# Kernel tuning notes

Hardware: AMD Instinct MI355X
Metric: run time of the kernel (lower is better)

Reference implementation:

```python
import jax, jax.numpy as jnp
import numpy as np

SL, BS, E, H, PF, STRIDE, SHIFT = 2048, 2, 1024, 16, 16, 1, 0
DH = E // H  # 64


def setup_inputs() -> dict:
    key = jax.random.key(0)
    ks = jax.random.split(key, 6)
    s = 0.02
    return {
        'x': jax.random.normal(ks[0], (SL, BS, E), jnp.float32),
        'ln_g': jnp.ones((E,), jnp.float32),
        'ln_b': jnp.zeros((E,), jnp.float32),
        'Wq': jax.random.normal(ks[1], (E, E), jnp.float32) * s,
        'bq': jnp.zeros((E,), jnp.float32),
        'Wk': jax.random.normal(ks[2], (E, E), jnp.float32) * s,
        'bk': jnp.zeros((E,), jnp.float32),
        'Wv': jax.random.normal(ks[3], (E, E), jnp.float32) * s,
        'bv': jnp.zeros((E,), jnp.float32),
        'Wo': jax.random.normal(ks[4], (E, E), jnp.float32) * s,
        'bo': jnp.zeros((E,), jnp.float32),
    }


def _layernorm(x, g, b, eps=1e-5):
    m = x.mean(-1, keepdims=True)
    v = jnp.var(x, axis=-1, keepdims=True)
    return (x - m) * jax.lax.rsqrt(v + eps) * g + b


def _sparsify(context, h):
    # faithful to sparsify(): r = (arange(h)+1)*stride - pf + shift (+ arange(pf)), mod c
    c = context.shape[0]
    base = (jnp.arange(h) + 1) * STRIDE - PF + SHIFT          # [h]
    idx = (base[None, :] + jnp.arange(PF)[:, None]) % c       # [pf, h]
    return context[idx.reshape(-1)].reshape(PF, h, context.shape[1], context.shape[2])


def reference(x, ln_g, ln_b, Wq, bq, Wk, bk, Wv, bv, Wo, bo):
    sl, bs, e = x.shape
    residual = x
    xn = _layernorm(x, ln_g, ln_b)
    # gather pf-sized local context window per query position (modular wrap)
    fetch = _sparsify(xn, sl)                                  # [pf, sl, bs, E]
    # per-token query (length-1) attending to its pf gathered keys
    q = (xn @ Wq + bq).reshape(sl, bs, H, DH)                  # [sl,bs,H,dh]
    k = (fetch @ Wk + bk).reshape(PF, sl, bs, H, DH)           # [pf,sl,bs,H,dh]
    v = (fetch @ Wv + bv).reshape(PF, sl, bs, H, DH)
    scale = 1.0 / jnp.sqrt(jnp.float32(DH))
    scores = jnp.einsum('sbhd,psbhd->sbhp', q, k) * scale      # [sl,bs,H,pf]
    attn = jax.nn.softmax(scores, axis=-1)
    out = jnp.einsum('sbhp,psbhd->sbhd', attn, v).reshape(sl, bs, e)
    out = out @ Wo + bo                                        # output projection
    # dropout is a no-op in eval
    return residual + out
```

## Files before the change

### kernel.cpp

```cpp
#include <hip/hip_runtime.h>
#include <cstdint>
#include <cstddef>

#define SLEN 2048
#define BSZ  2
#define EDIM 1024
#define NHEAD 16
#define DHEAD 64
#define PFW  16
#define NTOK (SLEN*BSZ)

#define BK 32

typedef __attribute__((ext_vector_type(8))) short short8;
typedef __attribute__((ext_vector_type(4))) float floatx4;
typedef __attribute__((ext_vector_type(4))) int   int4v;

__device__ __forceinline__ short f2bf(float f) {
  union { float f; uint32_t u; } v; v.f = f;
  uint32_t r = v.u + 0x7fffu + ((v.u >> 16) & 1u);
  return (short)(r >> 16);
}
__device__ __forceinline__ float bf2f(short s) {
  union { uint32_t u; float f; } v; v.u = ((uint32_t)(uint16_t)s) << 16;
  return v.f;
}
__device__ __forceinline__ int q8(float f, float inv) {
  int q = __float2int_rn(f * inv);
  return min(127, max(-127, q));
}

__device__ __forceinline__ void async16(const void* g, void* l) {
  __builtin_amdgcn_global_load_lds((const __attribute__((address_space(1))) void*)g,
                                   (__attribute__((address_space(3))) void*)l,
                                   16, 0, 0);
}

__global__ __launch_bounds__(256) void prep_kernel(
    const float* __restrict__ x, const float* __restrict__ g,
    const float* __restrict__ b, char* __restrict__ xn_i8,
    float* __restrict__ xn_scl,
    const float* __restrict__ W0, const float* __restrict__ W1,
    const float* __restrict__ W2, const float* __restrict__ W3,
    short* __restrict__ Wt_base)
{
  const int bid = blockIdx.x;
  const int tid = threadIdx.x;

  if (bid < NTOK) {
    const int row = bid;
    const float4 v = ((const float4*)(x + (size_t)row * EDIM))[tid];
    float s  = v.x + v.y + v.z + v.w;
    float ss = v.x * v.x + v.y * v.y + v.z * v.z + v.w * v.w;
#pragma unroll
    for (int off = 32; off; off >>= 1) {
      s  += __shfl_xor(s, off);
      ss += __shfl_xor(ss, off);
    }
    __shared__ float ws_s[4], ws_ss[4], ws_m[4];
    const int lane = tid & 63, wave = tid >> 6;
    if (lane == 0) { ws_s[wave] = s; ws_ss[wave] = ss; }
    __syncthreads();
    s  = ws_s[0] + ws_s[1] + ws_s[2] + ws_s[3];
    ss = ws_ss[0] + ws_ss[1] + ws_ss[2] + ws_ss[3];

    const float mean = s * (1.0f / EDIM);
    const float var  = ss * (1.0f / EDIM) - mean * mean;
    const float rs   = rsqrtf(var + 1e-5f);

    const float4 gv = ((const float4*)g)[tid];
    const float4 bv = ((const float4*)b)[tid];
    const float n0 = (v.x - mean) * rs * gv.x + bv.x;
    const float n1 = (v.y - mean) * rs * gv.y + bv.y;
    const float n2 = (v.z - mean) * rs * gv.z + bv.z;
    const float n3 = (v.w - mean) * rs * gv.w + bv.w;

    float am = fmaxf(fmaxf(fabsf(n0), fabsf(n1)), fmaxf(fabsf(n2), fabsf(n3)));
#pragma unroll
    for (int off = 32; off; off >>= 1) am = fmaxf(am, __shfl_xor(am, off));
    if (lane == 0) ws_m[wave] = am;
    __syncthreads();
    am = fmaxf(fmaxf(ws_m[0], ws_m[1]), fmaxf(ws_m[2], ws_m[3]));

    const float inv = (am > 1e-30f) ? 127.0f / am : 0.0f;
    const int q0 = q8(n0, inv), q1 = q8(n1, inv), q2 = q8(n2, inv), q3 = q8(n3, inv);
    const uint32_t pack = (uint32_t)(q0 & 0xff) | ((uint32_t)(q1 & 0xff) << 8) |
                          ((uint32_t)(q2 & 0xff) << 16) | ((uint32_t)(q3 & 0xff) << 24);
    ((uint32_t*)(xn_i8 + (size_t)row * EDIM))[tid] = pack;
    if (tid == 0) xn_scl[row] = am * (1.0f / 127.0f);
  } else {
    const int t = bid - NTOK;
    const int z = t >> 10;
    const int rem = t & 1023;
    const int n0 = (rem & 31) * 32;
    const int k0 = (rem >> 5) * 32;
    const float* W = (z == 0) ? W0 : (z == 1) ? W1 : (z == 2) ? W2 : W3;
    short* Wt = Wt_base + (size_t)z * EDIM * EDIM;

    __shared__ float tile[32][33];
    const int tx = tid & 31;
    const int ty = tid >> 5;
#pragma unroll
    for (int i = 0; i < 4; ++i)
      tile[ty + i * 8][tx] = W[(size_t)(k0 + ty + i * 8) * EDIM + n0 + tx];
    __syncthreads();
#pragma unroll
    for (int i = 0; i < 4; ++i)
      Wt[(size_t)(n0 + ty + i * 8) * EDIM + k0 + tx] = f2bf(tile[tx][ty + i * 8]);
  }
}

__global__ __launch_bounds__(256) void quant_w(
    const short* __restrict__ Wt, char* __restrict__ w_i8,
    float* __restrict__ w_scl)
{
  const int R = blockIdx.x;
  const int tid = threadIdx.x;
  const short4 s4 = ((const short4*)(Wt + (size_t)R * EDIM))[tid];
  const float w0 = bf2f(s4.x), w1 = bf2f(s4.y), w2 = bf2f(s4.z), w3 = bf2f(s4.w);

  float am = fmaxf(fmaxf(fabsf(w0), fabsf(w1)), fmaxf(fabsf(w2), fabsf(w3)));
#pragma unroll
  for (int off = 32; off; off >>= 1) am = fmaxf(am, __shfl_xor(am, off));
  __shared__ float wm[4];
  const int lane = tid & 63, wave = tid >> 6;
  if (lane == 0) wm[wave] = am;
  __syncthreads();
  am = fmaxf(fmaxf(wm[0], wm[1]), fmaxf(wm[2], wm[3]));

  const float inv = (am > 1e-30f) ? 127.0f / am : 0.0f;
  const int q0 = q8(w0, inv), q1 = q8(w1, inv), q2 = q8(w2, inv), q3 = q8(w3, inv);
  const uint32_t pack = (uint32_t)(q0 & 0xff) | ((uint32_t)(q1 & 0xff) << 8) |
                        ((uint32_t)(q2 & 0xff) << 16) | ((uint32_t)(q3 & 0xff) << 24);
  ((uint32_t*)(w_i8 + (size_t)R * EDIM))[tid] = pack;
  if (tid == 0) w_scl[R] = am * (1.0f / 127.0f);
}

__global__ __launch_bounds__(256) void gemm_qkv_i8(
    const char* __restrict__ xn_i8, const float* __restrict__ xn_scl,
    const char* __restrict__ w_i8, const float* __restrict__ w_scl,
    const float* __restrict__ bq, const float* __restrict__ bk,
    const float* __restrict__ bv, short* __restrict__ qkv_base)
{
  __shared__ __align__(16) char As[128 * 64];
  __shared__ __align__(16) char Bs[128 * 64];

  const int bid  = blockIdx.x;
  const int xcd  = bid & 7;
  const int slot = bid >> 3;
  const int nz   = xcd * 3 + slot / 32;
  const int mt   = slot & 31;
  const int z    = nz >> 3;
  const int nt   = nz & 7;

  const char*  Bt   = w_i8 + (size_t)z * EDIM * EDIM;
  const float* bscl = w_scl + z * EDIM;
  const float* bias = (z == 0) ? bq : (z == 1) ? bk : bv;
  short* out        = qkv_base + (size_t)z * NTOK * EDIM;

  const int bm = mt * 128;
  const int bn = nt * 128;
  const int tid  = threadIdx.x;
  const int lane = tid & 63;
  const int wave = tid >> 6;

  int4v acc[4][4];
#pragma unroll
  for (int i = 0; i < 4; ++i)
#pragma unroll
    for (int j = 0; j < 4; ++j) { int4v zz = {0, 0, 0, 0}; acc[i][j] = zz; }

  const int lrow  = lane >> 2;
  const int lcolB = (lane & 3) * 16;
  const char* gA0 = xn_i8 + (size_t)(bm + wave * 32 + lrow) * EDIM + lcolB;
  const char* gA1 = gA0 + (size_t)16 * EDIM;
  const char* gB0 = Bt + (size_t)(bn + wave * 32 + lrow) * EDIM + lcolB;
  const char* gB1 = gB0 + (size_t)16 * EDIM;
  char* lA0 = As + wave * 2048;
  char* lA1 = lA0 + 1024;
  char* lB0 = Bs + wave * 2048;
  char* lB1 = lB0 + 1024;

  const int wm  = (wave >> 1) * 64;
  const int wn  = (wave & 1) * 64;
  const int fr  = lane & 15;
  const int fqB = (lane >> 4) * 16;

  for (int k0 = 0; k0 < EDIM; k0 += 64) {
    async16(gA0, lA0); async16(gA1, lA1);
    async16(gB0, lB0); async16(gB1, lB1);
    gA0 += 64; gA1 += 64; gB0 += 64; gB1 += 64;
    __syncthreads();

    int4v af[4], bf[4];
#pragma unroll
    for (int mi = 0; mi < 4; ++mi)
      af[mi] = *(const int4v*)(As + (size_t)(wm + mi * 16 + fr) * 64 + fqB);
#pragma unroll
    for (int ni = 0; ni < 4; ++ni)
      bf[ni] = *(const int4v*)(Bs + (size_t)(wn + ni * 16 + fr) * 64 + fqB);
#pragma unroll
    for (int mi = 0; mi < 4; ++mi)
#pragma unroll
      for (int ni = 0; ni < 4; ++ni)
        acc[mi][ni] = __builtin_amdgcn_mfma_i32_16x16x64_i8(
            af[mi], bf[ni], acc[mi][ni], 0, 0, 0);
    __syncthreads();
  }

  const int r0 = bm + wm + ((lane >> 4) * 4);
  const int c0 = bn + wn + (lane & 15);
#pragma unroll
  for (int mi = 0; mi < 4; ++mi) {
    float sa[4];
#pragma unroll
    for (int r = 0; r < 4; ++r) sa[r] = xn_scl[r0 + mi * 16 + r];
#pragma unroll
    for (int ni = 0; ni < 4; ++ni) {
      const int4v v = acc[mi][ni];
      const int col = c0 + ni * 16;
      const float sb = bscl[col];
      const float bb = bias[col];
#pragma unroll
      for (int r = 0; r < 4; ++r) {
        const int row = r0 + mi * 16 + r;
        out[(size_t)row * EDIM + col] = f2bf((float)v[r] * (sa[r] * sb) + bb);
      }
    }
  }
}

__global__ __launch_bounds__(256) void gemm_o(
    const short* __restrict__ Aattn, const short* __restrict__ Wot,
    const float* __restrict__ bo, const float* __restrict__ residual,
    float* __restrict__ out)
{
  __shared__ short As[64 * BK];
  __shared__ short Bs[128 * BK];
  const int bm = blockIdx.x * 64;
  const int bn = blockIdx.y * 128;
  const int tid  = threadIdx.x;
  const int lane = tid & 63;
  const int wave = tid >> 6;

  floatx4 acc[2][4];
#pragma unroll
  for (int i = 0; i < 2; ++i)
#pragma unroll
    for (int j = 0; j < 4; ++j) { floatx4 zz = {0.f, 0.f, 0.f, 0.f}; acc[i][j] = zz; }

  const int lrow = lane >> 2;
  const int lcol = (lane & 3) * 8;
  const short* gA0 = Aattn + (size_t)(bm + wave * 16 + lrow) * EDIM + lcol;
  const short* gB0 = Wot + (size_t)(bn + wave * 32 + lrow) * EDIM + lcol;
  const short* gB1 = gB0 + (size_t)16 * EDIM;
  short* lA0 = As + wave * 512;
  short* lB0 = Bs + wave * 1024;
  short* lB1 = lB0 + 512;

  const int wm = (wave >> 1) * 32;
  const int wn = (wave & 1) * 64;
  const int fr = lane & 15;
  const int fq = (lane >> 4) * 8;

  for (int k0 = 0; k0 < EDIM; k0 += BK) {
    async16(gA0, lA0);
    async16(gB0, lB0); async16(gB1, lB1);
    gA0 += BK; gB0 += BK; gB1 += BK;
    __syncthreads();

    short8 af[2], bf[4];
#pragma unroll
    for (int mi = 0; mi < 2; ++mi)
      af[mi] = *(const short8*)(As + (size_t)(wm + mi * 16 + fr) * BK + fq);
#pragma unroll
    for (int ni = 0; ni < 4; ++ni)
      bf[ni] = *(const short8*)(Bs + (size_t)(wn + ni * 16 + fr) * BK + fq);
#pragma unroll
    for (int mi = 0; mi < 2; ++mi)
#pragma unroll
      for (int ni = 0; ni < 4; ++ni)
        acc[mi][ni] = __builtin_amdgcn_mfma_f32_16x16x32_bf16(
            af[mi], bf[ni], acc[mi][ni], 0, 0, 0);
    __syncthreads();
  }

  const int r0 = bm + wm + ((lane >> 4) * 4);
  const int c0 = bn + wn + (lane & 15);
#pragma unroll
  for (int mi = 0; mi < 2; ++mi)
#pragma unroll
    for (int ni = 0; ni < 4; ++ni) {
      const floatx4 v = acc[mi][ni];
      const int col = c0 + ni * 16;
      const float bb = bo[col];
#pragma unroll
      for (int r = 0; r < 4; ++r) {
        const int row = r0 + mi * 16 + r;
        const size_t idx = (size_t)row * EDIM + col;
        out[idx] = residual[idx] + v[r] + bb;
      }
    }
}

#define VT_LD 80
#define PB_LD 40

__global__ __launch_bounds__(256) void attn_mfma(
    const short* __restrict__ Q, const short* __restrict__ K,
    const short* __restrict__ V, short* __restrict__ O)
{
  const int tid  = threadIdx.x;
  const int lane = tid & 63;
  const int wave = tid >> 6;
  const int quad = lane >> 4;
  const int l16  = lane & 15;

  const int bh = blockIdx.y;
  const int h  = bh & (NHEAD - 1);
  const int b  = bh >> 4;
  const int s_blk = blockIdx.x * 64;
  const int col0  = h * DHEAD;

  __shared__ __align__(16) short VT[64 * VT_LD];
  __shared__ __align__(16) short Pb[4][16 * PB_LD];

  for (int task = tid; task < 320; task += 256) {
    const int kp  = task >> 3;
    const int dg  = task & 7;
    const int kk0 = kp * 2;
    int sA = s_blk - 15 + kk0;
    int sB = sA + 1;
    if (sA < 0) sA += SLEN;  if (sA >= SLEN) sA -= SLEN;
    if (sB < 0) sB += SLEN;  if (sB >= SLEN) sB -= SLEN;
    const short8 vA = *(const short8*)(V + (size_t)(sA * BSZ + b) * EDIM + col0 + dg * 8);
    const short8 vB = *(const short8*)(V + (size_t)(sB * BSZ + b) * EDIM + col0 + dg * 8);
#pragma unroll
    for (int j = 0; j < 8; ++j) {
      const int d = dg * 8 + j;
      const uint32_t pack = (uint32_t)(uint16_t)vA[j] | ((uint32_t)(uint16_t)vB[j] << 16);
      *(uint32_t*)&VT[d * VT_LD + kk0] = pack;
    }
  }

  const int sw = s_blk + wave * 16;
  short8 aq[2];
  {
    const size_t base = (size_t)((sw + l16) * BSZ + b) * EDIM + col0 + quad * 8;
    aq[0] = *(const short8*)(Q + base);
    aq[1] = *(const short8*)(Q + base + 32);
  }
  short8 bkf[2][2];
#pragma unroll
  for (int T = 0; T < 2; ++T) {
    int ks = sw - 15 + T * 16 + l16;
    if (ks < 0) ks += SLEN;
    if (ks >= SLEN) ks -= SLEN;
    const size_t base = (size_t)(ks * BSZ + b) * EDIM + col0 + quad * 8;
    bkf[T][0] = *(const short8*)(K + base);
    bkf[T][1] = *(const short8*)(K + base + 32);
  }

  floatx4 S[2];
  { floatx4 zz = {0.f, 0.f, 0.f, 0.f}; S[0] = zz; S[1] = zz; }
#pragma unroll
  for (int T = 0; T < 2; ++T) {
    S[T] = __builtin_amdgcn_mfma_f32_16x16x32_bf16(aq[0], bkf[T][0], S[T], 0, 0, 0);
    S[T] = __builtin_amdgcn_mfma_f32_16x16x32_bf16(aq[1], bkf[T][1], S[T], 0, 0, 0);
  }

  float sc[2][4];
#pragma unroll
  for (int T = 0; T < 2; ++T)
#pragma unroll
    for (int r = 0; r < 4; ++r) {
      const int m = quad * 4 + r;
      const int c = T * 16 + l16;
      const int d = c - m;
      sc[T][r] = (d >= 0 && d <= 15) ? S[T][r] * 0.125f : -1e30f;
    }
  float mx[4], sm[4];
#pragma unroll
  for (int r = 0; r < 4; ++r) mx[r] = fmaxf(sc[0][r], sc[1][r]);
#pragma unroll
  for (int off = 1; off <= 8; off <<= 1)
#pragma unroll
    for (int r = 0; r < 4; ++r) mx[r] = fmaxf(mx[r], __shfl_xor(mx[r], off));
  float p[2][4];
#pragma unroll
  for (int r = 0; r < 4; ++r) {
    p[0][r] = __expf(sc[0][r] - mx[r]);
    p[1][r] = __expf(sc[1][r] - mx[r]);
    sm[r] = p[0][r] + p[1][r];
  }
#pragma unroll
  for (int off = 1; off <= 8; off <<= 1)
#pragma unroll
    for (int r = 0; r < 4; ++r) sm[r] += __shfl_xor(sm[r], off);

  __syncthreads();

  short* Pw = Pb[wave];
#pragma unroll
  for (int T = 0; T < 2; ++T)
#pragma unroll
    for (int r = 0; r < 4; ++r) {
      const int m = quad * 4 + r;
      const int c = T * 16 + l16;
      Pw[m * PB_LD + c] = f2bf(p[T][r]);
    }
  __syncthreads();
  const short8 ap = *(const short8*)(Pw + l16 * PB_LD + quad * 8);

  floatx4 Oacc[4];
  { floatx4 zz = {0.f, 0.f, 0.f, 0.f}; Oacc[0] = zz; Oacc[1] = zz; Oacc[2] = zz; Oacc[3] = zz; }
#pragma unroll
  for (int nt = 0; nt < 4; ++nt) {
    const short8 bv = *(const short8*)(VT + (nt * 16 + l16) * VT_LD + wave * 16 + quad * 8);
    Oacc[nt] = __builtin_amdgcn_mfma_f32_16x16x32_bf16(ap, bv, Oacc[nt], 0, 0, 0);
  }

#pragma unroll
  for (int nt = 0; nt < 4; ++nt)
#pragma unroll
    for (int r = 0; r < 4; ++r) {
      const int m = quad * 4 + r;
      const size_t idx = (size_t)((sw + m) * BSZ + b) * EDIM + col0 + nt * 16 + l16;
      O[idx] = f2bf(Oacc[nt][r] / sm[r]);
    }
}

extern "C" void kernel_launch(void* const* d_in, const int* in_sizes, int n_in,
                              void* d_out, int out_size, void* d_ws, size_t ws_size,
                              hipStream_t stream) {
  const float* x    = (const float*)d_in[0];
  const float* ln_g = (const float*)d_in[1];
  const float* ln_b = (const float*)d_in[2];
  const float* Wq   = (const float*)d_in[3];
  const float* bq   = (const float*)d_in[4];
  const float* Wk   = (const float*)d_in[5];
  const float* bk   = (const float*)d_in[6];
  const float* Wv   = (const float*)d_in[7];
  const float* bv   = (const float*)d_in[8];
  const float* Wo   = (const float*)d_in[9];
  const float* bo   = (const float*)d_in[10];
  float* out = (float*)d_out;

  char* ws = (char*)d_ws;
  char*  xn_i8  = ws;
  short* Wt     = (short*)(ws + ((size_t)4  << 20));
  char*  w_i8   = ws + ((size_t)12 << 20);
  short* QKV    = (short*)(ws + ((size_t)15 << 20));
  short* attn   = (short*)(ws + ((size_t)39 << 20));
  float* xn_scl = (float*)(ws + ((size_t)47 << 20));
  float* w_scl  = (float*)(ws + ((size_t)47 << 20) + (1 << 16));

  prep_kernel<<<NTOK + 4096, 256, 0, stream>>>(x, ln_g, ln_b, xn_i8, xn_scl,
                                               Wq, Wk, Wv, Wo, Wt);
  quant_w<<<3 * EDIM, 256, 0, stream>>>(Wt, w_i8, w_scl);
  gemm_qkv_i8<<<768, 256, 0, stream>>>(xn_i8, xn_scl, w_i8, w_scl,
                                       bq, bk, bv, QKV);
  attn_mfma<<<dim3(SLEN / 64, BSZ * NHEAD), 256, 0, stream>>>(
      QKV, QKV + (size_t)NTOK * EDIM, QKV + (size_t)2 * NTOK * EDIM, attn);
  gemm_o<<<dim3(NTOK / 64, EDIM / 128), 256, 0, stream>>>(
      attn, Wt + (size_t)3 * EDIM * EDIM, bo, x, out);
}
```

Before: 153.3 us.

## Quantize attention output to int8 and run output projection with int8 MFMA

The attention kernel now emits per-row, per-head int8 values plus a scale, instead of bf16. The output projection becomes an int8 GEMM using i32 MFMA with a K-tile of 64, which matches one head. Each tile's integer partial is rescaled into a float accumulator, and the quantization of Wo is folded into the existing weight quantizer by extending its grid. The aim is to halve operand bytes and use the faster int8 matrix path, at the cost of extra per-tile dequantization work and lower accuracy.

```diff
diff --git a/kernel.cpp b/kernel.cpp
--- a/kernel.cpp
+++ b/kernel.cpp
@@ -230,75 +230,100 @@
   }
 }
 
-__global__ __launch_bounds__(256) void gemm_o(
-    const short* __restrict__ Aattn, const short* __restrict__ Wot,
+__global__ __launch_bounds__(256) void gemm_o_i8(
+    const char* __restrict__ A8, const float* __restrict__ a_scl,
+    const char* __restrict__ w_i8, const float* __restrict__ w_scl,
     const float* __restrict__ bo, const float* __restrict__ residual,
     float* __restrict__ out)
 {
-  __shared__ short As[64 * BK];
-  __shared__ short Bs[128 * BK];
+  __shared__ __align__(16) char As[64 * 64];
+  __shared__ __align__(16) char Bs[128 * 64];
+  __shared__ float sa_lds[64 * 17];
+
   const int bm = blockIdx.x * 64;
   const int bn = blockIdx.y * 128;
   const int tid  = threadIdx.x;
   const int lane = tid & 63;
   const int wave = tid >> 6;
 
-  floatx4 acc[2][4];
+#pragma unroll
+  for (int i = 0; i < 4; ++i) {
+    const int e = tid + i * 256;
+    const int row = e >> 4, h = e & 15;
+    sa_lds[row * 17 + h] = a_scl[(size_t)(bm + row) * NHEAD + h];
+  }
+
+  floatx4 facc[2][4];
 #pragma unroll
   for (int i = 0; i < 2; ++i)
 #pragma unroll
-    for (int j = 0; j < 4; ++j) { floatx4 zz = {0.f, 0.f, 0.f, 0.f}; acc[i][j] = zz; }
-
-  const int lrow = lane >> 2;
-  const int lcol = (lane & 3) * 8;
-  const short* gA0 = Aattn + (size_t)(bm + wave * 16 + lrow) * EDIM + lcol;
-  const short* gB0 = Wot + (size_t)(bn + wave * 32 + lrow) * EDIM + lcol;
-  const short* gB1 = gB0 + (size_t)16 * EDIM;
-  short* lA0 = As + wave * 512;
-  short* lB0 = Bs + wave * 1024;
-  short* lB1 = lB0 + 512;
-
-  const int wm = (wave >> 1) * 32;
-  const int wn = (wave & 1) * 64;
-  const int fr = lane & 15;
-  const int fq = (lane >> 4) * 8;
-
-  for (int k0 = 0; k0 < EDIM; k0 += BK) {
+    for (int j = 0; j < 4; ++j) { floatx4 zz = {0.f, 0.f, 0.f, 0.f}; facc[i][j] = zz; }
+
+  const int lrow  = lane >> 2;
+  const int lcolB = (lane & 3) * 16;
+  const char* gA0 = A8 + (size_t)(bm + wave * 16 + lrow) * EDIM + lcolB;
+  const char* gB0 = w_i8 + (size_t)3 * EDIM * EDIM +
+                    (size_t)(bn + wave * 32 + lrow) * EDIM + lcolB;
+  const char* gB1 = gB0 + (size_t)16 * EDIM;
+  char* lA0 = As + wave * 1024;
+  char* lB0 = Bs + wave * 2048;
+  char* lB1 = lB0 + 1024;
+
+  const int wm  = (wave >> 1) * 32;
+  const int wn  = (wave & 1) * 64;
+  const int fr  = lane & 15;
+  const int fqB = (lane >> 4) * 16;
+  const int q4  = lane >> 4;
+
+  for (int ki = 0; ki < 16; ++ki) {
     async16(gA0, lA0);
     async16(gB0, lB0); async16(gB1, lB1);
-    gA0 += BK; gB0 += BK; gB1 += BK;
-    __syncthreads();
-
-    short8 af[2], bf[4];
+    gA0 += 64; gB0 += 64; gB1 += 64;
+    __syncthreads();
+
+    int4v af[2], bf[4];
 #pragma unroll
     for (int mi = 0; mi < 2; ++mi)
-      af[mi] = *(const short8*)(As + (size_t)(wm + mi * 16 + fr) * BK + fq);
+      af[mi] = *(const int4v*)(As + (size_t)(wm + mi * 16 + fr) * 64 + fqB);
 #pragma unroll
     for (int ni = 0; ni < 4; ++ni)
-      bf[ni] = *(const short8*)(Bs + (size_t)(wn + ni * 16 + fr) * BK + fq);
+      bf[ni] = *(const int4v*)(Bs + (size_t)(wn + ni * 16 + fr) * 64 + fqB);
+
+    float sa_v[2][4];
 #pragma unroll
     for (int mi = 0; mi < 2; ++mi)
 #pragma unroll
-      for (int ni = 0; ni < 4; ++ni)
-        acc[mi][ni] = __builtin_amdgcn_mfma_f32_16x16x32_bf16(
-            af[mi], bf[ni], acc[mi][ni], 0, 0, 0);
-    __syncthreads();
-  }
-
-  const int r0 = bm + wm + ((lane >> 4) * 4);
+      for (int r = 0; r < 4; ++r)
+        sa_v[mi][r] = sa_lds[(wm + mi * 16 + q4 * 4 + r) * 17 + ki];
+
+#pragma unroll
+    for (int mi = 0; mi < 2; ++mi)
+#pragma unroll
+      for (int ni = 0; ni < 4; ++ni) {
+        const int4v zz = {0, 0, 0, 0};
+        const int4v t = __builtin_amdgcn_mfma_i32_16x16x64_i8(
+            af[mi], bf[ni], zz, 0, 0, 0);
+#pragma unroll
+        for (int r = 0; r < 4; ++r)
+          facc[mi][ni][r] += sa_v[mi][r] * (float)t[r];
+      }
+    __syncthreads();
+  }
+
+  const int r0 = bm + wm + q4 * 4;
   const int c0 = bn + wn + (lane & 15);
 #pragma unroll
   for (int mi = 0; mi < 2; ++mi)
 #pragma unroll
     for (int ni = 0; ni < 4; ++ni) {
-      const floatx4 v = acc[mi][ni];
       const int col = c0 + ni * 16;
+      const float sb = w_scl[3 * EDIM + col];
       const float bb = bo[col];
 #pragma unroll
       for (int r = 0; r < 4; ++r) {
         const int row = r0 + mi * 16 + r;
         const size_t idx = (size_t)row * EDIM + col;
-        out[idx] = residual[idx] + v[r] + bb;
+        out[idx] = residual[idx] + facc[mi][ni][r] * sb + bb;
       }
     }
 }
@@ -308,7 +333,8 @@
 
 __global__ __launch_bounds__(256) void attn_mfma(
     const short* __restrict__ Q, const short* __restrict__ K,
-    const short* __restrict__ V, short* __restrict__ O)
+    const short* __restrict__ V, char* __restrict__ O8,
+    float* __restrict__ a_scl)
 {
   const int tid  = threadIdx.x;
   const int lane = tid & 63;
@@ -420,14 +446,41 @@
     Oacc[nt] = __builtin_amdgcn_mfma_f32_16x16x32_bf16(ap, bv, Oacc[nt], 0, 0, 0);
   }
 
+  float vv[4][4];
+  float am[4] = {0.f, 0.f, 0.f, 0.f};
+#pragma unroll
+  for (int nt = 0; nt < 4; ++nt)
+#pragma unroll
+    for (int r = 0; r < 4; ++r) {
+      const float v = Oacc[nt][r] / sm[r];
+      vv[nt][r] = v;
+      am[r] = fmaxf(am[r], fabsf(v));
+    }
+#pragma unroll
+  for (int off = 1; off <= 8; off <<= 1)
+#pragma unroll
+    for (int r = 0; r < 4; ++r) am[r] = fmaxf(am[r], __shfl_xor(am[r], off));
+
+  float inv[4];
+#pragma unroll
+  for (int r = 0; r < 4; ++r) inv[r] = (am[r] > 1e-30f) ? 127.0f / am[r] : 0.0f;
+
 #pragma unroll
   for (int nt = 0; nt < 4; ++nt)
 #pragma unroll
     for (int r = 0; r < 4; ++r) {
       const int m = quad * 4 + r;
-      const size_t idx = (size_t)((sw + m) * BSZ + b) * EDIM + col0 + nt * 16 + l16;
-      O[idx] = f2bf(Oacc[nt][r] / sm[r]);
-    }
+      const int row = (sw + m) * BSZ + b;
+      O8[(size_t)row * EDIM + col0 + nt * 16 + l16] = (char)q8(vv[nt][r], inv[r]);
+    }
+  if (l16 == 0) {
+#pragma unroll
+    for (int r = 0; r < 4; ++r) {
+      const int m = quad * 4 + r;
+      const int row = (sw + m) * BSZ + b;
+      a_scl[(size_t)row * NHEAD + h] = am[r] * (1.0f / 127.0f);
+    }
+  }
 }
 
 extern "C" void kernel_launch(void* const* d_in, const int* in_sizes, int n_in,
@@ -447,21 +500,23 @@
   float* out = (float*)d_out;
 
   char* ws = (char*)d_ws;
-  char*  xn_i8  = ws;
-  short* Wt     = (short*)(ws + ((size_t)4  << 20));
-  char*  w_i8   = ws + ((size_t)12 << 20);
-  short* QKV    = (short*)(ws + ((size_t)15 << 20));
-  short* attn   = (short*)(ws + ((size_t)39 << 20));
-  float* xn_scl = (float*)(ws + ((size_t)47 << 20));
-  float* w_scl  = (float*)(ws + ((size_t)47 << 20) + (1 << 16));
+  char*  xn_i8   = ws;
+  short* Wt      = (short*)(ws + ((size_t)4  << 20));
+  char*  w_i8    = ws + ((size_t)12 << 20);
+  short* QKV     = (short*)(ws + ((size_t)16 << 20));
+  char*  attn_i8 = ws + ((size_t)40 << 20);
+  float* xn_scl  = (float*)(ws + ((size_t)44 << 20));
+  float* w_scl   = (float*)(ws + ((size_t)44 << 20) + (1 << 16));
+  float* a_scl   = (float*)(ws + ((size_t)44 << 20) + (2 << 16));
 
   prep_kernel<<<NTOK + 4096, 256, 0, stream>>>(x, ln_g, ln_b, xn_i8, xn_scl,
                                                Wq, Wk, Wv, Wo, Wt);
-  quant_w<<<3 * EDIM, 256, 0, stream>>>(Wt, w_i8, w_scl);
+  quant_w<<<4 * EDIM, 256, 0, stream>>>(Wt, w_i8, w_scl);
   gemm_qkv_i8<<<768, 256, 0, stream>>>(xn_i8, xn_scl, w_i8, w_scl,
                                        bq, bk, bv, QKV);
   attn_mfma<<<dim3(SLEN / 64, BSZ * NHEAD), 256, 0, stream>>>(
-      QKV, QKV + (size_t)NTOK * EDIM, QKV + (size_t)2 * NTOK * EDIM, attn);
-  gemm_o<<<dim3(NTOK / 64, EDIM / 128), 256, 0, stream>>>(
-      attn, Wt + (size_t)3 * EDIM * EDIM, bo, x, out);
-}
+      QKV, QKV + (size_t)NTOK * EDIM, QKV + (size_t)2 * NTOK * EDIM,
+      attn_i8, a_scl);
+  gemm_o_i8<<<dim3(NTOK / 64, EDIM / 128), 256, 0, stream>>>(
+      attn_i8, a_scl, w_i8, w_scl, bo, x, out);
+}
```

New measurement: 152.4 us. No clear change (-0.6%).
